# Performance work log

Hardware: AMD Instinct MI355X
Metric: run time of the kernel (lower is better)

## Reference

```python
import jax, jax.numpy as jnp
import numpy as np

BN_EPS = 1e-5

def _l2norm(x, axis):
    # F.normalize: x / max(||x||_2, 1e-12)
    n = jnp.sqrt(jnp.sum(x * x, axis=axis, keepdims=True))
    return x / jnp.maximum(n, 1e-12)

def _psi(x_bhc, w, g, b):
    # 1x1 conv over HW-as-channels: [B,HW,C] x [D,HW] -> [B,D,C]
    y = jnp.einsum('dh,bhc->bdc', w, x_bhc)
    # inference BatchNorm2d with running_mean=0, running_var=1
    scale = g / jnp.sqrt(1.0 + BN_EPS)
    y = y * scale[None, :, None] + b[None, :, None]
    return jax.nn.relu(y)

def setup_inputs() -> dict:
    key = jax.random.key(0)
    ks = jax.random.split(key, 8)
    B, C, H, W, D = 16, 2048, 32, 32, 256
    return {
        'v2l_conv_feature': jax.random.normal(ks[0], (B, C, H, W), jnp.float32),
        'l2v_conv_feature': jax.random.normal(ks[1], (B, C, H, W), jnp.float32),
        'w_v2l': jax.random.normal(ks[2], (D, H * W), jnp.float32) * 0.02,
        'g_v2l': jax.random.uniform(ks[3], (D,), jnp.float32, 0.5, 1.5),
        'b_v2l': jax.random.normal(ks[4], (D,), jnp.float32) * 0.1,
        'w_l2v': jax.random.normal(ks[5], (D, H * W), jnp.float32) * 0.02,
        'g_l2v': jax.random.uniform(ks[6], (D,), jnp.float32, 0.5, 1.5),
        'b_l2v': jax.random.normal(ks[7], (D,), jnp.float32) * 0.1,
    }

def reference(v2l_conv_feature, l2v_conv_feature, w_v2l, g_v2l, b_v2l, w_l2v, g_l2v, b_l2v):
    B, C, H, W = v2l_conv_feature.shape
    HW = H * W
    xv = jnp.transpose(v2l_conv_feature.reshape(B, C, HW), (0, 2, 1))  # [B,HW,C]
    xl = jnp.transpose(l2v_conv_feature.reshape(B, C, HW), (0, 2, 1))  # [B,HW,C]
    v2l_adj = _l2norm(_psi(xv, w_v2l, g_v2l, b_v2l), axis=2)  # [B,D,C], norm over C
    l2v_adj = _l2norm(_psi(xl, w_l2v, g_l2v, b_l2v), axis=1)  # [B,D,C], norm over D
    # Faithful to torch: reshape of the permuted tensor is a raw row-major
    # reinterpretation [B,HW,C] -> [B,C,HW] (NOT a transpose back).
    xv_r = xv.reshape(B, C, HW)
    latent = jnp.einsum('bdc,bch->bdh', v2l_adj, xv_r)          # [B,D,HW]
    latent_n = _l2norm(latent, axis=-1)
    aff = jax.nn.softmax(jnp.einsum('bdh,beh->bde', latent_n, latent_n), axis=-1)  # [B,D,D]
    latent = jnp.einsum('bde,beh->bdh', aff, latent)            # [B,D,HW]
    visible = jnp.einsum('bdc,bdh->bch', l2v_adj, latent)       # [B,C,HW]
    return visible.reshape(B, C, H, W)
```

## Files before the change

kernel.cpp:

```cpp
#include <hip/hip_runtime.h>
#include <hip/hip_bf16.h>

#define BB 16
#define CC 2048
#define HWW 1024
#define DD 256
#define BN_RSQRT 0.9999950000374997f

typedef short bf16x8 __attribute__((ext_vector_type(8)));
typedef float f32x4 __attribute__((ext_vector_type(4)));
typedef unsigned short u16x8 __attribute__((ext_vector_type(8)));
typedef unsigned short u16x4 __attribute__((ext_vector_type(4)));
typedef unsigned short u16;

typedef __attribute__((address_space(1))) const unsigned GU;
typedef __attribute__((address_space(3))) unsigned LU;
__device__ __forceinline__ void gload16(const void* g, void* l) {
    __builtin_amdgcn_global_load_lds((GU*)g, (LU*)l, 16, 0, 0);
}

__device__ __forceinline__ unsigned short f2bf(float x) {
    unsigned u = __builtin_bit_cast(unsigned, x);
    unsigned r = u + 0x7FFFu + ((u >> 16) & 1u);
    return (unsigned short)(r >> 16);
}
__device__ __forceinline__ float bf2f(unsigned short h) {
    unsigned u = ((unsigned)h) << 16;
    return __builtin_bit_cast(float, u);
}
__device__ __forceinline__ void split2(float x, unsigned short& hi, unsigned short& lo) {
    hi = f2bf(x);
    lo = f2bf(x - bf2f(hi));
}

struct RegsA { u16x8 h[2]; u16x8 l[2]; };
struct RegsB { u16x8 h[2]; u16x8 l[2]; };

__global__ __launch_bounds__(256) void split_k(const float* __restrict__ in,
                                               u16* __restrict__ hi, u16* __restrict__ lo,
                                               long long n8) {
    long long i = (long long)blockIdx.x * 256 + threadIdx.x;
    if (i >= n8) return;
    const float4* p = (const float4*)in + i * 2;
    float4 a = p[0], b = p[1];
    float xs[8] = {a.x, a.y, a.z, a.w, b.x, b.y, b.z, b.w};
    u16x8 h, l;
    #pragma unroll
    for (int j = 0; j < 8; ++j) { unsigned short hh, ll; split2(xs[j], hh, ll); h[j] = hh; l[j] = ll; }
    *(u16x8*)(hi + i * 8) = h;
    *(u16x8*)(lo + i * 8) = l;
}

template <int BF, int EPI, int FUSE2, int KS>
__global__ __launch_bounds__(512, 4) void gemm2b(
    const u16* __restrict__ Ah0, const u16* __restrict__ Al0,
    const u16* __restrict__ Ah1, const u16* __restrict__ Al1,
    long long aB, int lda,
    const void* __restrict__ B0a, const void* __restrict__ B0b,
    const void* __restrict__ B1a, const void* __restrict__ B1b,
    long long bB, int ldb,
    float* __restrict__ C0, float* __restrict__ C1,
    long long cB, long long kB, int ldc,
    int K,
    const float* __restrict__ g0, const float* __restrict__ bb0,
    const float* __restrict__ g1, const float* __restrict__ bb1)
{
    __shared__ __attribute__((aligned(16))) char smem[2][32768];

    const int gx = gridDim.x, gy = gridDim.y;
    int nwg = gx * gy * gridDim.z;
    int id = blockIdx.x + gx * (blockIdx.y + gy * blockIdx.z);
    int chunk = nwg >> 3;
    int nid = (id & 7) * chunk + (id >> 3);
    int bx = nid % gx;
    int tmp = nid / gx;
    int by = tmp % gy;
    int bz = tmp / gy;

    const int t = threadIdx.x;
    const int n0 = bx * 128, m0 = by * 128;

    int op = 0, batch, kz = 0;
    if constexpr (FUSE2) { op = bz >> 4; batch = bz & 15; }
    else if constexpr (KS > 1) { batch = bz / KS; kz = bz - batch * KS; }
    else { batch = bz; }
    const int koffA = kz * K;

    const u16* Ahp = (op ? Ah1 : Ah0) + (long long)batch * aB + koffA;
    const u16* Alp = (op ? Al1 : Al0) + (long long)batch * aB + koffA;
    const float* Bf = nullptr;
    const u16* Bh = nullptr;
    const u16* Bl = nullptr;
    if constexpr (BF == 0) {
        Bf = (const float*)(op ? B1a : B0a) + (long long)batch * bB;
        Bf += ((long long)(koffA >> 10)) * 1024 * ldb + (koffA & 1023);
    } else {
        Bh = (const u16*)(op ? B1a : B0a) + (long long)batch * bB;
        Bl = (const u16*)(op ? B1b : B0b) + (long long)batch * bB;
    }
    float* Cb = ((EPI == 1 && FUSE2) ? (op ? C1 : C0) : C0)
              + (long long)batch * cB + (long long)kz * kB;
    const float* gp = op ? g1 : g0;
    const float* bp = op ? bb1 : bb0;

    const int arow = t >> 2;
    const int aslt = (t & 3) ^ ((t >> 3) & 3);
    const int bswz = (t & 3) ^ ((arow >> 1) & 3);

    const int l = t & 63, w = t >> 6;
    const int wr = w >> 2, wc = w & 3;
    const int rl = l & 15, kq = l >> 4;
    const int fsw = (kq ^ ((rl >> 1) & 3)) * 16;

    f32x4 acc[4][2];
    #pragma unroll
    for (int i = 0; i < 4; ++i)
        #pragma unroll
        for (int j = 0; j < 2; ++j)
            acc[i][j] = (f32x4){0.f, 0.f, 0.f, 0.f};

    float4 rb0, rb1;

    auto loadBregs = [&](int k0) {
        if constexpr (BF == 0) {
            const float* p = Bf + (long long)(n0 + arow) * ldb + k0 + (t & 3) * 8;
            rb0 = *(const float4*)p;
            rb1 = *(const float4*)(p + 4);
        }
    };
    auto gstage = [&](int k0, char* sn) {
        const u16* pa = Ahp + (long long)(m0 + arow) * lda + k0 + aslt * 8;
        gload16(pa, sn + t * 16);
        const u16* pl = Alp + (long long)(m0 + arow) * lda + k0 + aslt * 8;
        gload16(pl, sn + 8192 + t * 16);
        if constexpr (BF == 1) {
            const u16* pbh = Bh + (long long)(n0 + arow) * ldb + k0 + aslt * 8;
            gload16(pbh, sn + 16384 + t * 16);
            const u16* pbl = Bl + (long long)(n0 + arow) * ldb + k0 + aslt * 8;
            gload16(pbl, sn + 24576 + t * 16);
        }
    };
    auto splitWriteB = [&](char* sn) {
        if constexpr (BF == 0) {
            float xs[8] = {rb0.x, rb0.y, rb0.z, rb0.w, rb1.x, rb1.y, rb1.z, rb1.w};
            u16x8 h, lo;
            #pragma unroll
            for (int e = 0; e < 8; ++e) {
                unsigned short hh, ll; split2(xs[e], hh, ll);
                h[e] = hh; lo[e] = ll;
            }
            char* base = sn + 16384 + arow * 64 + bswz * 16;
            *(u16x8*)(base) = h;
            *(u16x8*)(base + 8192) = lo;
        }
    };

    auto readA = [&](const char* sb, bf16x8* fah, bf16x8* fal) {
        #pragma unroll
        for (int i2 = 0; i2 < 4; ++i2) {
            int off = (wr * 64 + i2 * 16 + rl) * 64 + fsw;
            fah[i2] = *(const bf16x8*)(sb + off);
            fal[i2] = *(const bf16x8*)(sb + 8192 + off);
        }
    };
    auto readB = [&](const char* sb, bf16x8* fbh, bf16x8* fbl) {
        #pragma unroll
        for (int j = 0; j < 2; ++j) {
            int off = (wc * 32 + j * 16 + rl) * 64 + fsw;
            fbh[j] = *(const bf16x8*)(sb + 16384 + off);
            fbl[j] = *(const bf16x8*)(sb + 24576 + off);
        }
    };

    const int NIT = K >> 5;

    loadBregs(0);
    gstage(0, smem[0]);
    if constexpr (BF == 0) {
        asm volatile("s_waitcnt vmcnt(2)" ::: "memory");
        splitWriteB(smem[0]);
    }
    asm volatile("s_waitcnt vmcnt(0)" ::: "memory");
    asm volatile("s_waitcnt lgkmcnt(0)" ::: "memory");
    __builtin_amdgcn_s_barrier();

    for (int it = 0; it < NIT; ++it) {
        char* sb = smem[it & 1];
        char* sn = smem[(it + 1) & 1];
        const bool more = (it + 1) < NIT;
        if (more) { loadBregs((it + 1) << 5); gstage((it + 1) << 5, sn); }

        bf16x8 fah[4], fal[4], fbh[2], fbl[2];
        readB(sb, fbh, fbl);
        readA(sb, fah, fal);

        if (more && BF == 0) {
            asm volatile("s_waitcnt vmcnt(2)" ::: "memory");
            splitWriteB(sn);
        }

        __builtin_amdgcn_s_setprio(1);
        #pragma unroll
        for (int i2 = 0; i2 < 4; ++i2)
            #pragma unroll
            for (int j = 0; j < 2; ++j)
                acc[i2][j] = __builtin_amdgcn_mfma_f32_16x16x32_bf16(fal[i2], fbh[j], acc[i2][j], 0, 0, 0);
        #pragma unroll
        for (int i2 = 0; i2 < 4; ++i2)
            #pragma unroll
            for (int j = 0; j < 2; ++j)
                acc[i2][j] = __builtin_amdgcn_mfma_f32_16x16x32_bf16(fah[i2], fbl[j], acc[i2][j], 0, 0, 0);
        #pragma unroll
        for (int i2 = 0; i2 < 4; ++i2)
            #pragma unroll
            for (int j = 0; j < 2; ++j)
                acc[i2][j] = __builtin_amdgcn_mfma_f32_16x16x32_bf16(fah[i2], fbh[j], acc[i2][j], 0, 0, 0);
        __builtin_amdgcn_s_setprio(0);

        if (more) { asm volatile("s_waitcnt vmcnt(0)" ::: "memory"); }
        asm volatile("s_waitcnt lgkmcnt(0)" ::: "memory");
        __builtin_amdgcn_s_barrier();
    }

    #pragma unroll
    for (int i = 0; i < 4; ++i) {
        #pragma unroll
        for (int r = 0; r < 4; ++r) {
            int row = m0 + wr * 64 + i * 16 + kq * 4 + r;
            float sc = 1.0f, bi = 0.0f;
            if (EPI == 1) { sc = gp[row] * BN_RSQRT; bi = bp[row]; }
            #pragma unroll
            for (int j = 0; j < 2; ++j) {
                int col = n0 + wc * 32 + j * 16 + rl;
                float v = acc[i][j][r];
                if (EPI == 1) v = fmaxf(fmaf(v, sc, bi), 0.0f);
                Cb[(long long)row * ldc + col] = v;
            }
        }
    }
}

template <int BN_, int EPI>
__global__ __launch_bounds__(256) void mfma_gemm(
    const void* __restrict__ Ap, const void* __restrict__ Ap2, long long aB, int lda,
    const void* __restrict__ Bp, const void* __restrict__ Bp2, long long bB, int ldb,
    void* __restrict__ Cp, void* __restrict__ Cp2,
    long long cB, int ldc, int K)
{
    constexpr int NJ   = BN_ / 32;
    constexpr int BNB  = BN_ * 64;
    constexpr int BUFB = 16384 + BN_ * 128;
    __shared__ __attribute__((aligned(16))) char smem[2][BUFB];

    const int gx = gridDim.x, gy = gridDim.y;
    int nwg = gx * gy * gridDim.z;
    int id = blockIdx.x + gx * (blockIdx.y + gy * blockIdx.z);
    int chunk = nwg >> 3;
    int nid = (id & 7) * chunk + (id >> 3);
    int bx = nid % gx;
    int tmp = nid / gx;
    int by = tmp % gy;
    int bz = tmp / gy;

    const int t  = threadIdx.x;
    const int n0 = bx * BN_;
    const int m0 = by * 128;

    const int ar = t >> 1, ag = t & 1;
    const int af = (ar >> 1) & 3;
    const int as0 = (2 * ag) ^ af, as1 = (2 * ag + 1) ^ af;
    const bool bact = (BN_ == 128) || (t < 2 * BN_);
    const int br = (t >> 1) & (BN_ - 1), bg = t & 1;
    const int bf = (br >> 1) & 3;
    const int bs0 = (2 * bg) ^ bf, bs1 = (2 * bg + 1) ^ bf;

    const int l  = t & 63, w = t >> 6;
    const int wr = w >> 1, wc = w & 1;
    const int rl = l & 15, kq = l >> 4;
    const int sw = kq ^ ((rl >> 1) & 3);
    const int aoff = (wr * 64 + rl) * 64 + sw * 16;
    const int boff = (wc * (BN_ / 2) + rl) * 64 + sw * 16;

    const u16* Ahp = (const u16*)Ap  + (long long)bz * aB;
    const u16* Alp = (const u16*)Ap2 + (long long)bz * aB;
    const u16* Bhp = (const u16*)Bp  + (long long)bz * bB;
    const u16* Blp = (const u16*)Bp2 + (long long)bz * bB;

    auto loadA = [&](int k0, RegsA& ra) {
        const u16* ph = Ahp + (long long)(m0 + ar) * lda + k0 + ag * 16;
        const u16* pl = Alp + (long long)(m0 + ar) * lda + k0 + ag * 16;
        ra.h[0] = *(const u16x8*)(ph);
        ra.h[1] = *(const u16x8*)(ph + 8);
        ra.l[0] = *(const u16x8*)(pl);
        ra.l[1] = *(const u16x8*)(pl + 8);
    };
    auto loadB = [&](int k0, RegsB& rb) {
        if (!bact) return;
        const u16* ph = Bhp + (long long)(n0 + br) * ldb + k0 + bg * 16;
        const u16* pl = Blp + (long long)(n0 + br) * ldb + k0 + bg * 16;
        rb.h[0] = *(const u16x8*)(ph);
        rb.h[1] = *(const u16x8*)(ph + 8);
        rb.l[0] = *(const u16x8*)(pl);
        rb.l[1] = *(const u16x8*)(pl + 8);
    };
    auto stageWrite = [&](char* sb, RegsA& ra, RegsB& rb) {
        *(u16x8*)(sb + ar * 64 + as0 * 16) = ra.h[0];
        *(u16x8*)(sb + ar * 64 + as1 * 16) = ra.h[1];
        *(u16x8*)(sb + 8192 + ar * 64 + as0 * 16) = ra.l[0];
        *(u16x8*)(sb + 8192 + ar * 64 + as1 * 16) = ra.l[1];
        if (bact) {
            char* sB = sb + 16384;
            *(u16x8*)(sB + br * 64 + bs0 * 16) = rb.h[0];
            *(u16x8*)(sB + br * 64 + bs1 * 16) = rb.h[1];
            *(u16x8*)(sB + BNB + br * 64 + bs0 * 16) = rb.l[0];
            *(u16x8*)(sB + BNB + br * 64 + bs1 * 16) = rb.l[1];
        }
    };

    f32x4 acc[4][NJ];
    #pragma unroll
    for (int i = 0; i < 4; ++i)
        #pragma unroll
        for (int j = 0; j < NJ; ++j)
            acc[i][j] = (f32x4){0.f, 0.f, 0.f, 0.f};

    RegsA a0, a1;
    RegsB b0, b1;
    const int NIT = K >> 5;

    loadA(0, a0); loadB(0, b0);
    stageWrite(smem[0], a0, b0);
    loadA(32, a1); loadB(32, b1);
    asm volatile("s_waitcnt lgkmcnt(0)" ::: "memory");
    __builtin_amdgcn_s_barrier();

    auto step = [&](int it, char* sb, char* sn, RegsA& pa, RegsB& pb,
                    RegsA& qa, RegsB& qb) {
        bf16x8 fah[4], fal[4], fbh[NJ], fbl[NJ];
        #pragma unroll
        for (int i = 0; i < 4; ++i) {
            fah[i] = *(const bf16x8*)(sb + aoff + i * 1024);
            fal[i] = *(const bf16x8*)(sb + 8192 + aoff + i * 1024);
        }
        #pragma unroll
        for (int j = 0; j < NJ; ++j) {
            fbh[j] = *(const bf16x8*)(sb + 16384 + boff + j * 1024);
            fbl[j] = *(const bf16x8*)(sb + 16384 + BNB + boff + j * 1024);
        }
        if (it + 1 < NIT) stageWrite(sn, pa, pb);
        if (it + 2 < NIT) { loadA((it + 2) << 5, qa); loadB((it + 2) << 5, qb); }
        #pragma unroll
        for (int i = 0; i < 4; ++i)
            #pragma unroll
            for (int j = 0; j < NJ; ++j) {
                acc[i][j] = __builtin_amdgcn_mfma_f32_16x16x32_bf16(fal[i], fbh[j], acc[i][j], 0, 0, 0);
                acc[i][j] = __builtin_amdgcn_mfma_f32_16x16x32_bf16(fah[i], fbl[j], acc[i][j], 0, 0, 0);
                acc[i][j] = __builtin_amdgcn_mfma_f32_16x16x32_bf16(fah[i], fbh[j], acc[i][j], 0, 0, 0);
            }
        asm volatile("s_waitcnt lgkmcnt(0)" ::: "memory");
        __builtin_amdgcn_s_barrier();
    };

    for (int it = 0; it < NIT; it += 2) {
        step(it,     smem[0], smem[1], a1, b1, a0, b0);
        step(it + 1, smem[1], smem[0], a0, b0, a1, b1);
    }

    #pragma unroll
    for (int i = 0; i < 4; ++i) {
        #pragma unroll
        for (int r = 0; r < 4; ++r) {
            int row = m0 + wr * 64 + i * 16 + kq * 4 + r;
            #pragma unroll
            for (int j = 0; j < NJ; ++j) {
                int col = n0 + wc * (BN_ / 2) + j * 16 + rl;
                float v = acc[i][j][r];
                if constexpr (EPI == 0) {
                    ((float*)Cp + (long long)bz * cB)[(long long)row * ldc + col] = v;
                } else {
                    unsigned short hh, ll; split2(v, hh, ll);
                    ((u16*)Cp  + (long long)bz * cB)[(long long)row * ldc + col] = hh;
                    ((u16*)Cp2 + (long long)bz * cB)[(long long)row * ldc + col] = ll;
                }
            }
        }
    }
}

__global__ __launch_bounds__(256) void rownorm_split_perm_k(float* __restrict__ Y) {
    int d = blockIdx.x, b = blockIdx.y, t = threadIdx.x;
    float* row = Y + ((long long)b * DD + d) * CC;
    float4 v0 = ((const float4*)row)[2 * t];
    float4 v1 = ((const float4*)row)[2 * t + 1];
    float s = v0.x * v0.x + v0.y * v0.y + v0.z * v0.z + v0.w * v0.w
            + v1.x * v1.x + v1.y * v1.y + v1.z * v1.z + v1.w * v1.w;
    for (int off = 32; off > 0; off >>= 1) s += __shfl_down(s, off, 64);
    __shared__ float wsum[4];
    __shared__ float ivs;
    int lane = t & 63, w = t >> 6;
    if (lane == 0) wsum[w] = s;
    __syncthreads();
    if (t == 0) ivs = 1.0f / fmaxf(sqrtf(wsum[0] + wsum[1] + wsum[2] + wsum[3]), 1e-12f);
    __syncthreads();
    float iv = ivs;
    float xs[8] = {v0.x * iv, v0.y * iv, v0.z * iv, v0.w * iv,
                   v1.x * iv, v1.y * iv, v1.z * iv, v1.w * iv};
    u16x4 he, ho, le, lo4;
    #pragma unroll
    for (int j = 0; j < 4; ++j) {
        unsigned short hh, ll;
        split2(xs[2 * j], hh, ll);       he[j] = hh; le[j] = ll;
        split2(xs[2 * j + 1], hh, ll);   ho[j] = hh; lo4[j] = ll;
    }
    u16* hi = (u16*)row;
    *(u16x4*)(hi + 4 * t) = he;
    *(u16x4*)(hi + 1024 + 4 * t) = ho;
    *(u16x4*)(hi + 2048 + 4 * t) = le;
    *(u16x4*)(hi + 3072 + 4 * t) = lo4;
}

__global__ __launch_bounds__(256) void transnorm_k(const float* __restrict__ Yl,
                                                   u16* __restrict__ hi, u16* __restrict__ lo) {
    __shared__ float tile[256][33];
    __shared__ float part[8][33];
    __shared__ float invn[32];
    int c0 = blockIdx.x * 32, b = blockIdx.y;
    int t = threadIdx.x;
    int tx = t & 31, ty = t >> 5;
    const float* base = Yl + (long long)b * DD * CC + c0;
    for (int d = ty; d < 256; d += 8)
        tile[d][tx] = base[(long long)d * CC + tx];
    __syncthreads();
    float s = 0.0f;
    #pragma unroll
    for (int dd = 0; dd < 32; ++dd) {
        float v = tile[ty * 32 + dd][tx];
        s += v * v;
    }
    part[ty][tx] = s;
    __syncthreads();
    if (ty == 0) {
        float tot = part[0][tx] + part[1][tx] + part[2][tx] + part[3][tx]
                  + part[4][tx] + part[5][tx] + part[6][tx] + part[7][tx];
        invn[tx] = 1.0f / fmaxf(sqrtf(tot), 1e-12f);
    }
    __syncthreads();
    long long ob = (long long)b * DD * CC;
    #pragma unroll 4
    for (int i = 0; i < 32; ++i) {
        float v = tile[t][i] * invn[i];
        unsigned short hh, ll; split2(v, hh, ll);
        long long o = ob + (long long)(c0 + i) * DD + t;
        hi[o] = hh; lo[o] = ll;
    }
}

__global__ __launch_bounds__(256) void latreduce_k(const float* __restrict__ parts,
                                                   u16* __restrict__ hi, u16* __restrict__ lo,
                                                   u16* __restrict__ thi, u16* __restrict__ tlo) {
    __shared__ float tile[32][33];
    int h0 = blockIdx.x * 32, d0 = blockIdx.y * 32, b = blockIdx.z;
    const long long sL = (long long)DD * HWW;
    const long long ps = (long long)BB * sL;
    const float* base = parts + (long long)b * sL;
    int tx = threadIdx.x & 31, ty = threadIdx.x >> 5;
    for (int i = ty; i < 32; i += 8) {
        long long o = (long long)(d0 + i) * HWW + h0 + tx;
        float s = base[o] + base[o + ps];
        tile[i][tx] = s;
        unsigned short hh, ll; split2(s, hh, ll);
        long long od = (long long)b * sL + o;
        hi[od] = hh; lo[od] = ll;
    }
    __syncthreads();
    for (int i = ty; i < 32; i += 8) {
        float v = tile[tx][i];
        unsigned short hh, ll; split2(v, hh, ll);
        long long ot = (long long)b * sL + (long long)(h0 + i) * DD + d0 + tx;
        thi[ot] = hh; tlo[ot] = ll;
    }
}

__global__ __launch_bounds__(256) void latnorm_k(const float* __restrict__ G,
                                                 float* __restrict__ rs) {
    int i = blockIdx.x * 256 + threadIdx.x;
    int b = i >> 8, d = i & 255;
    float v = G[((long long)b * DD + d) * DD + d];
    rs[i] = 1.0f / fmaxf(sqrtf(v), 1e-12f);
}

__global__ __launch_bounds__(256) void softmax_k(const float* __restrict__ G,
                                                 const float* __restrict__ rs,
                                                 u16* __restrict__ affHi,
                                                 u16* __restrict__ affLo) {
    int d = blockIdx.x, b = blockIdx.y;
    const float* row = G + ((long long)b * DD + d) * DD;
    const float* rsb = rs + (long long)b * DD;
    int t = threadIdx.x;
    float lg = row[t] * rsb[d] * rsb[t];

    float m = lg;
    for (int off = 32; off > 0; off >>= 1) m = fmaxf(m, __shfl_down(m, off, 64));
    __shared__ float wsm[4];
    __shared__ float bm, bs;
    int lane = t & 63, w = t >> 6;
    if (lane == 0) wsm[w] = m;
    __syncthreads();
    if (t == 0) bm = fmaxf(fmaxf(wsm[0], wsm[1]), fmaxf(wsm[2], wsm[3]));
    __syncthreads();
    float e = expf(lg - bm);
    float s = e;
    for (int off = 32; off > 0; off >>= 1) s += __shfl_down(s, off, 64);
    if (lane == 0) wsm[w] = s;
    __syncthreads();
    if (t == 0) bs = wsm[0] + wsm[1] + wsm[2] + wsm[3];
    __syncthreads();
    float v = e / bs;
    unsigned short hh, ll; split2(v, hh, ll);
    long long o = ((long long)b * DD + d) * DD + t;
    affHi[o] = hh; affLo[o] = ll;
}

extern "C" void kernel_launch(void* const* d_in, const int* in_sizes, int n_in,
                              void* d_out, int out_size, void* d_ws, size_t ws_size,
                              hipStream_t stream) {
    const float* v2l   = (const float*)d_in[0];
    const float* l2v   = (const float*)d_in[1];
    const float* w_v2l = (const float*)d_in[2];
    const float* g_v2l = (const float*)d_in[3];
    const float* b_v2l = (const float*)d_in[4];
    const float* w_l2v = (const float*)d_in[5];
    const float* g_l2v = (const float*)d_in[6];
    const float* b_l2v = (const float*)d_in[7];
    float* out = (float*)d_out;

    char* W = (char*)d_ws;
    float* Yv     = (float*)(W + 0);
    float* Yl     = (float*)(W + 33554432);
    u16*   YltHi  = (u16*)(W + 67108864);
    u16*   YltLo  = (u16*)(W + 83886080);
    u16*   latHi  = (u16*)(W + 100663296);
    u16*   latLo  = (u16*)(W + 109051904);
    u16*   latTHi = (u16*)(W + 117440512);
    u16*   latTLo = (u16*)(W + 125829120);
    u16*   l2tHi  = (u16*)(W + 134217728);
    u16*   l2tLo  = (u16*)(W + 142606336);
    float* gram   = (float*)(W + 150994944);
    float* rs     = (float*)(W + 155189248);
    u16*   affHi  = (u16*)(W + 155336704);
    u16*   affLo  = (u16*)(W + 157433856);
    u16*   WvHi   = (u16*)(W + 159531008);
    u16*   WvLo   = WvHi + 262144;
    u16*   WlHi   = WvLo + 262144;
    u16*   WlLo   = WlHi + 262144;

    float* latPart = (float*)d_out;

    const long long sY   = (long long)DD * CC;
    const long long sL   = (long long)DD * HWW;
    const long long sG   = (long long)DD * DD;
    const long long sX   = (long long)CC * HWW;
    const long long sYp  = (long long)DD * 4096;

    split_k<<<128, 256, 0, stream>>>(w_v2l, WvHi, WvLo, 32768);
    split_k<<<128, 256, 0, stream>>>(w_l2v, WlHi, WlLo, 32768);

    gemm2b<0, 1, 1, 1><<<dim3(CC / 128, DD / 128, 32), 512, 0, stream>>>(
        WvHi, WvLo, WlHi, WlLo, 0, HWW,
        v2l, nullptr, l2v, nullptr, sX, HWW,
        Yv, Yl, sY, 0, CC, HWW,
        g_v2l, b_v2l, g_l2v, b_l2v);

    rownorm_split_perm_k<<<dim3(DD, BB), 256, 0, stream>>>(Yv);
    transnorm_k<<<dim3(CC / 32, BB), 256, 0, stream>>>(Yl, YltHi, YltLo);

    gemm2b<0, 0, 0, 2><<<dim3(HWW / 128, DD / 128, 32), 512, 0, stream>>>(
        (const u16*)Yv, (const u16*)Yv + 2048, nullptr, nullptr, sYp, 4096,
        v2l, nullptr, nullptr, nullptr, sX, HWW,
        latPart, nullptr, sL, (long long)BB * sL, HWW, 1024,
        nullptr, nullptr, nullptr, nullptr);

    latreduce_k<<<dim3(HWW / 32, DD / 32, BB), 256, 0, stream>>>(
        latPart, latHi, latLo, latTHi, latTLo);

    mfma_gemm<64, 0><<<dim3(4, 2, BB), 256, 0, stream>>>(
        latHi, latLo, sL, HWW, latHi, latLo, sL, HWW,
        gram, nullptr, sG, DD, HWW);

    latnorm_k<<<dim3(BB * DD / 256), 256, 0, stream>>>(gram, rs);
    softmax_k<<<dim3(DD, BB), 256, 0, stream>>>(gram, rs, affHi, affLo);

    mfma_gemm<128, 2><<<dim3(2, 8, BB), 256, 0, stream>>>(
        latTHi, latTLo, sL, DD, affHi, affLo, sG, DD,
        l2tHi, l2tLo, sL, DD, DD);

    gemm2b<1, 0, 0, 1><<<dim3(HWW / 128, CC / 128, BB), 512, 0, stream>>>(
        YltHi, YltLo, nullptr, nullptr, sY, DD,
        l2tHi, l2tLo, nullptr, nullptr, sL, DD,
        out, nullptr, sX, 0, HWW, DD,
        nullptr, nullptr, nullptr, nullptr);
}
```

Before: 345.7 us.

## Use 4-wave 128x128 GEMM tiles with 64x64 per-wave outputs and 4-way split-K

```diff
diff --git a/kernel.cpp b/kernel.cpp
--- a/kernel.cpp
+++ b/kernel.cpp
@@ -52,7 +52,7 @@
 }
 
 template <int BF, int EPI, int FUSE2, int KS>
-__global__ __launch_bounds__(512, 4) void gemm2b(
+__global__ __launch_bounds__(256, 2) void gemm4w(
     const u16* __restrict__ Ah0, const u16* __restrict__ Al0,
     const u16* __restrict__ Ah1, const u16* __restrict__ Al1,
     long long aB, int lda,
@@ -103,55 +103,71 @@
     const float* gp = op ? g1 : g0;
     const float* bp = op ? bb1 : bb0;
 
-    const int arow = t >> 2;
+    const int ar4 = t >> 2;
     const int aslt = (t & 3) ^ ((t >> 3) & 3);
-    const int bswz = (t & 3) ^ ((arow >> 1) & 3);
+    const int brow = t >> 1, bg = t & 1;
+    const int bfb = (brow >> 1) & 3;
+    const int bs0 = ((2 * bg) ^ bfb) * 16, bs1 = ((2 * bg + 1) ^ bfb) * 16;
 
     const int l = t & 63, w = t >> 6;
-    const int wr = w >> 2, wc = w & 3;
+    const int wr = w >> 1, wc = w & 1;
     const int rl = l & 15, kq = l >> 4;
     const int fsw = (kq ^ ((rl >> 1) & 3)) * 16;
 
-    f32x4 acc[4][2];
+    f32x4 acc[4][4];
     #pragma unroll
     for (int i = 0; i < 4; ++i)
         #pragma unroll
-        for (int j = 0; j < 2; ++j)
+        for (int j = 0; j < 4; ++j)
             acc[i][j] = (f32x4){0.f, 0.f, 0.f, 0.f};
 
-    float4 rb0, rb1;
+    float4 rb0, rb1, rb2, rb3;
 
     auto loadBregs = [&](int k0) {
         if constexpr (BF == 0) {
-            const float* p = Bf + (long long)(n0 + arow) * ldb + k0 + (t & 3) * 8;
-            rb0 = *(const float4*)p;
+            const float* p = Bf + (long long)(n0 + brow) * ldb + k0 + bg * 16;
+            rb0 = *(const float4*)(p);
             rb1 = *(const float4*)(p + 4);
+            rb2 = *(const float4*)(p + 8);
+            rb3 = *(const float4*)(p + 12);
         }
     };
     auto gstage = [&](int k0, char* sn) {
-        const u16* pa = Ahp + (long long)(m0 + arow) * lda + k0 + aslt * 8;
-        gload16(pa, sn + t * 16);
-        const u16* pl = Alp + (long long)(m0 + arow) * lda + k0 + aslt * 8;
-        gload16(pl, sn + 8192 + t * 16);
+        const u16* pa = Ahp + (long long)(m0 + ar4) * lda + k0 + aslt * 8;
+        gload16(pa,                       sn + t * 16);
+        gload16(pa + (long long)64 * lda, sn + 4096 + t * 16);
+        const u16* pl = Alp + (long long)(m0 + ar4) * lda + k0 + aslt * 8;
+        gload16(pl,                       sn + 8192 + t * 16);
+        gload16(pl + (long long)64 * lda, sn + 12288 + t * 16);
         if constexpr (BF == 1) {
-            const u16* pbh = Bh + (long long)(n0 + arow) * ldb + k0 + aslt * 8;
-            gload16(pbh, sn + 16384 + t * 16);
-            const u16* pbl = Bl + (long long)(n0 + arow) * ldb + k0 + aslt * 8;
-            gload16(pbl, sn + 24576 + t * 16);
+            const u16* pbh = Bh + (long long)(n0 + ar4) * ldb + k0 + aslt * 8;
+            gload16(pbh,                       sn + 16384 + t * 16);
+            gload16(pbh + (long long)64 * ldb, sn + 20480 + t * 16);
+            const u16* pbl = Bl + (long long)(n0 + ar4) * ldb + k0 + aslt * 8;
+            gload16(pbl,                       sn + 24576 + t * 16);
+            gload16(pbl + (long long)64 * ldb, sn + 28672 + t * 16);
         }
     };
     auto splitWriteB = [&](char* sn) {
         if constexpr (BF == 0) {
-            float xs[8] = {rb0.x, rb0.y, rb0.z, rb0.w, rb1.x, rb1.y, rb1.z, rb1.w};
-            u16x8 h, lo;
+            float xs[16] = {rb0.x, rb0.y, rb0.z, rb0.w, rb1.x, rb1.y, rb1.z, rb1.w,
+                            rb2.x, rb2.y, rb2.z, rb2.w, rb3.x, rb3.y, rb3.z, rb3.w};
+            u16x8 h0, h1, l0, l1;
             #pragma unroll
             for (int e = 0; e < 8; ++e) {
                 unsigned short hh, ll; split2(xs[e], hh, ll);
-                h[e] = hh; lo[e] = ll;
+                h0[e] = hh; l0[e] = ll;
             }
-            char* base = sn + 16384 + arow * 64 + bswz * 16;
-            *(u16x8*)(base) = h;
-            *(u16x8*)(base + 8192) = lo;
+            #pragma unroll
+            for (int e = 0; e < 8; ++e) {
+                unsigned short hh, ll; split2(xs[8 + e], hh, ll);
+                h1[e] = hh; l1[e] = ll;
+            }
+            char* base = sn + 16384 + brow * 64;
+            *(u16x8*)(base + bs0) = h0;
+            *(u16x8*)(base + bs1) = h1;
+            *(u16x8*)(base + 8192 + bs0) = l0;
+            *(u16x8*)(base + 8192 + bs1) = l1;
         }
     };
 
@@ -165,8 +181,8 @@
     };
     auto readB = [&](const char* sb, bf16x8* fbh, bf16x8* fbl) {
         #pragma unroll
-        for (int j = 0; j < 2; ++j) {
-            int off = (wc * 32 + j * 16 + rl) * 64 + fsw;
+        for (int j = 0; j < 4; ++j) {
+            int off = (wc * 64 + j * 16 + rl) * 64 + fsw;
             fbh[j] = *(const bf16x8*)(sb + 16384 + off);
             fbl[j] = *(const bf16x8*)(sb + 24576 + off);
         }
@@ -175,9 +191,10 @@
     const int NIT = K >> 5;
 
     loadBregs(0);
+    asm volatile("" ::: "memory");
     gstage(0, smem[0]);
     if constexpr (BF == 0) {
-        asm volatile("s_waitcnt vmcnt(2)" ::: "memory");
+        asm volatile("s_waitcnt vmcnt(4)" ::: "memory");
         splitWriteB(smem[0]);
     }
     asm volatile("s_waitcnt vmcnt(0)" ::: "memory");
@@ -188,14 +205,18 @@
         char* sb = smem[it & 1];
         char* sn = smem[(it + 1) & 1];
         const bool more = (it + 1) < NIT;
-        if (more) { loadBregs((it + 1) << 5); gstage((it + 1) << 5, sn); }
-
-        bf16x8 fah[4], fal[4], fbh[2], fbl[2];
+        if (more) {
+            loadBregs((it + 1) << 5);
+            asm volatile("" ::: "memory");
+            gstage((it + 1) << 5, sn);
+        }
+
+        bf16x8 fah[4], fal[4], fbh[4], fbl[4];
         readB(sb, fbh, fbl);
         readA(sb, fah, fal);
 
         if (more && BF == 0) {
-            asm volatile("s_waitcnt vmcnt(2)" ::: "memory");
+            asm volatile("s_waitcnt vmcnt(4)" ::: "memory");
             splitWriteB(sn);
         }
 
@@ -203,17 +224,17 @@
         #pragma unroll
         for (int i2 = 0; i2 < 4; ++i2)
             #pragma unroll
-            for (int j = 0; j < 2; ++j)
+            for (int j = 0; j < 4; ++j)
                 acc[i2][j] = __builtin_amdgcn_mfma_f32_16x16x32_bf16(fal[i2], fbh[j], acc[i2][j], 0, 0, 0);
         #pragma unroll
         for (int i2 = 0; i2 < 4; ++i2)
             #pragma unroll
-            for (int j = 0; j < 2; ++j)
+            for (int j = 0; j < 4; ++j)
                 acc[i2][j] = __builtin_amdgcn_mfma_f32_16x16x32_bf16(fah[i2], fbl[j], acc[i2][j], 0, 0, 0);
         #pragma unroll
         for (int i2 = 0; i2 < 4; ++i2)
             #pragma unroll
-            for (int j = 0; j < 2; ++j)
+            for (int j = 0; j < 4; ++j)
                 acc[i2][j] = __builtin_amdgcn_mfma_f32_16x16x32_bf16(fah[i2], fbh[j], acc[i2][j], 0, 0, 0);
         __builtin_amdgcn_s_setprio(0);
 
@@ -230,8 +251,8 @@
             float sc = 1.0f, bi = 0.0f;
             if (EPI == 1) { sc = gp[row] * BN_RSQRT; bi = bp[row]; }
             #pragma unroll
-            for (int j = 0; j < 2; ++j) {
-                int col = n0 + wc * 32 + j * 16 + rl;
+            for (int j = 0; j < 4; ++j) {
+                int col = n0 + wc * 64 + j * 16 + rl;
                 float v = acc[i][j][r];
                 if (EPI == 1) v = fmaxf(fmaf(v, sc, bi), 0.0f);
                 Cb[(long long)row * ldc + col] = v;
@@ -466,7 +487,7 @@
     int tx = threadIdx.x & 31, ty = threadIdx.x >> 5;
     for (int i = ty; i < 32; i += 8) {
         long long o = (long long)(d0 + i) * HWW + h0 + tx;
-        float s = base[o] + base[o + ps];
+        float s = base[o] + base[o + ps] + base[o + 2 * ps] + base[o + 3 * ps];
         tile[i][tx] = s;
         unsigned short hh, ll; split2(s, hh, ll);
         long long od = (long long)b * sL + o;
@@ -565,7 +586,7 @@
     split_k<<<128, 256, 0, stream>>>(w_v2l, WvHi, WvLo, 32768);
     split_k<<<128, 256, 0, stream>>>(w_l2v, WlHi, WlLo, 32768);
 
-    gemm2b<0, 1, 1, 1><<<dim3(CC / 128, DD / 128, 32), 512, 0, stream>>>(
+    gemm4w<0, 1, 1, 1><<<dim3(CC / 128, DD / 128, 32), 256, 0, stream>>>(
         WvHi, WvLo, WlHi, WlLo, 0, HWW,
         v2l, nullptr, l2v, nullptr, sX, HWW,
         Yv, Yl, sY, 0, CC, HWW,
@@ -574,10 +595,10 @@
     rownorm_split_perm_k<<<dim3(DD, BB), 256, 0, stream>>>(Yv);
     transnorm_k<<<dim3(CC / 32, BB), 256, 0, stream>>>(Yl, YltHi, YltLo);
 
-    gemm2b<0, 0, 0, 2><<<dim3(HWW / 128, DD / 128, 32), 512, 0, stream>>>(
+    gemm4w<0, 0, 0, 4><<<dim3(HWW / 128, DD / 128, 64), 256, 0, stream>>>(
         (const u16*)Yv, (const u16*)Yv + 2048, nullptr, nullptr, sYp, 4096,
         v2l, nullptr, nullptr, nullptr, sX, HWW,
-        latPart, nullptr, sL, (long long)BB * sL, HWW, 1024,
+        latPart, nullptr, sL, (long long)BB * sL, HWW, 512,
         nullptr, nullptr, nullptr, nullptr);
 
     latreduce_k<<<dim3(HWW / 32, DD / 32, BB), 256, 0, stream>>>(
@@ -594,7 +615,7 @@
         latTHi, latTLo, sL, DD, affHi, affLo, sG, DD,
         l2tHi, l2tLo, sL, DD, DD);
 
-    gemm2b<1, 0, 0, 1><<<dim3(HWW / 128, CC / 128, BB), 512, 0, stream>>>(
+    gemm4w<1, 0, 0, 1><<<dim3(HWW / 128, CC / 128, BB), 256, 0, stream>>>(
         YltHi, YltLo, nullptr, nullptr, sY, DD,
         l2tHi, l2tLo, nullptr, nullptr, sL, DD,
         out, nullptr, sX, 0, HWW, DD,
```

New measurement: 370.4 us. +7.2%, slower.
